# Performance work log

Measured on AMD Instinct MI355X. Metric: run time of the kernel, lower is better.

Reference implementation:

```python
import jax, jax.numpy as jnp
import numpy as np

N_NODES = 100000
N_EDGES = 1000000
N_LABEL = 200000
D_IN = 128
D_HID = 128


def setup_inputs() -> dict:
    key = jax.random.key(0)
    k1, k2, k3, k4, k5 = jax.random.split(key, 5)
    node_feature = jax.random.normal(k1, (N_NODES, D_IN), dtype=jnp.float32)
    edge_index = jax.random.randint(k2, (2, N_EDGES), 0, N_NODES, dtype=jnp.int64)
    edge_label_index = jax.random.randint(k3, (2, N_LABEL), 0, N_NODES, dtype=jnp.int64)
    W1 = jax.random.normal(k4, (D_IN, D_HID), dtype=jnp.float32) * (1.0 / np.sqrt(D_IN))
    b1 = jnp.zeros((D_HID,), dtype=jnp.float32)
    W2 = jax.random.normal(k5, (D_HID, D_HID), dtype=jnp.float32) * (1.0 / np.sqrt(D_HID))
    b2 = jnp.zeros((D_HID,), dtype=jnp.float32)
    return {"node_feature": node_feature, "edge_index": edge_index,
            "edge_label_index": edge_label_index,
            "W1": W1, "b1": b1, "W2": W2, "b2": b2}


def reference(node_feature, edge_index, edge_label_index, W1, b1, W2, b2):
    N = node_feature.shape[0]
    # GCN normalization with added self-loops (PyG GCNConv default)
    loop = jnp.arange(N, dtype=edge_index.dtype)
    src = jnp.concatenate([edge_index[0], loop])  # [E+N]
    dst = jnp.concatenate([edge_index[1], loop])  # [E+N]
    deg = jax.ops.segment_sum(jnp.ones_like(dst, dtype=node_feature.dtype), dst, N)
    dinv = jnp.where(deg > 0, jax.lax.rsqrt(deg), 0.0)
    norm = dinv[src] * dinv[dst]  # [E+N]

    def gcn_conv(x, W, b):
        h = x @ W                              # [N, d] transform first (d small)
        msg = h[src] * norm[:, None]           # gather + scale over edges
        return jax.ops.segment_sum(msg, dst, N) + b  # scatter-add to targets

    # eval mode: dropout(p=0.2) is identity
    x = jax.nn.relu(gcn_conv(node_feature, W1, b1))
    x = gcn_conv(x, W2, b2)

    # edge scoring: gather both endpoints, elementwise mul, sum over features
    nodes_first = x[edge_label_index[0]]
    nodes_second = x[edge_label_index[1]]
    pred = jnp.sum(nodes_first * nodes_second, axis=-1)  # [N_LABEL]
    return pred
```

## Files before the change

### kernel.cpp

```cpp
#include <hip/hip_runtime.h>
#include <hip/hip_bf16.h>


#define N_NODES 100000
#define N_EDGES 1000000
#define N_LABEL 200000
#define D_FEAT 128
#define BM 128

#define NB 782
#define BCAP 2048
#define P1_EPT 16
#define P1_BLOCKS 245
#define G_GEMM 782
#define G_CONV 128

typedef short bf16x8 __attribute__((ext_vector_type(8)));
typedef float f32x4 __attribute__((ext_vector_type(4)));

__device__ inline unsigned int f2bf(float x) {
    unsigned int u = __float_as_uint(x);
    return (u + 0x7FFFu + ((u >> 16) & 1u)) >> 16;
}
__device__ inline unsigned int bf16pack(float a, float b) {
    return f2bf(a) | (f2bf(b) << 16);
}
__device__ inline float bflo(unsigned int u) { return __uint_as_float(u << 16); }
__device__ inline float bfhi(unsigned int u) { return __uint_as_float(u & 0xFFFF0000u); }

__global__ __launch_bounds__(256) void w2bf_pass1(
    const float* __restrict__ W1, const float* __restrict__ W2,
    unsigned short* __restrict__ Wt1, unsigned short* __restrict__ Wt2,
    const int* __restrict__ src, const int* __restrict__ dst,
    unsigned int* __restrict__ temp, int* __restrict__ bofs) {
    __shared__ __align__(16) unsigned int S[4096 + 1024 + 256];
    int b = blockIdx.x, t = threadIdx.x;
    if (b < G_CONV) {
        int i = b * 256 + t;
        const float* W = (i < 16384) ? W1 : W2;
        unsigned short* Wt = (i < 16384) ? Wt1 : Wt2;
        int j = i & 16383;
        int n = j >> 7, k = j & 127;
        Wt[j] = (unsigned short)f2bf(W[(size_t)k * 128 + n]);
        return;
    }
    b -= G_CONV;
    unsigned int* ed16 = S;
    int* hist = (int*)(ed16 + 4096);
    int* red = hist + 1024;

    for (int i = t; i < 1024; i += 256) hist[i] = 0;
    __syncthreads();

    int se[P1_EPT], de[P1_EPT], rk[P1_EPT];
    int e0 = b * 4096 + t;
#pragma unroll
    for (int j = 0; j < P1_EPT; ++j) {
        int e = e0 + j * 256;
        if (e < N_EDGES) {
            se[j] = src[e];
            de[j] = dst[e];
            rk[j] = atomicAdd(&hist[de[j] >> 7], 1);
        }
    }
    __syncthreads();

    int c0 = hist[4 * t], c1 = hist[4 * t + 1], c2 = hist[4 * t + 2], c3 = hist[4 * t + 3];
    int s = c0 + c1 + c2 + c3;
    red[t] = s;
    __syncthreads();
    for (int off = 1; off < 256; off <<= 1) {
        int a = (t >= off) ? red[t - off] : 0;
        __syncthreads();
        red[t] += a;
        __syncthreads();
    }
    int excl = red[t] - s;
    hist[4 * t] = excl;
    hist[4 * t + 1] = excl + c0;
    hist[4 * t + 2] = excl + c0 + c1;
    hist[4 * t + 3] = excl + c0 + c1 + c2;
    __syncthreads();

#pragma unroll
    for (int j = 0; j < P1_EPT; ++j) {
        int e = e0 + j * 256;
        if (e < N_EDGES) {
            int pos = hist[de[j] >> 7] + rk[j];
            ed16[pos] = (unsigned int)(((de[j] & 127) << 17) | se[j]);
        }
    }
    __syncthreads();

#pragma unroll
    for (int i = 0; i < 4; ++i)
        ((uint4*)temp)[(size_t)b * 1024 + i * 256 + t] = ((uint4*)ed16)[i * 256 + t];
    for (int j = t; j < NB; j += 256) bofs[b * (NB + 1) + j] = hist[j];
    if (t == 0) {
        int cnt = N_EDGES - b * 4096;
        if (cnt > 4096) cnt = 4096;
        bofs[b * (NB + 1) + NB] = cnt;
    }
}

template <bool BF16_IN>
__device__ __forceinline__ void gemm_body(const void* __restrict__ Xv,
                                          const unsigned short* __restrict__ Wt,
                                          unsigned int* __restrict__ Y,
                                          int nrows, int bid, short* Ws) {
    int t = threadIdx.x;
#pragma unroll
    for (int i = 0; i < 8; ++i) {
        int c = i * 256 + t;
        int n = c >> 4, q = c & 15;
        uint4 v = *(const uint4*)&Wt[(size_t)n * 128 + q * 8];
        *(uint4*)&Ws[n * 128 + ((q ^ (n & 15)) << 3)] = v;
    }
    __syncthreads();

    int wv = t >> 6;
    int lane = t & 63, l16 = lane & 15, quad = lane >> 4;
    int rbase = bid * BM + wv * 32;

    f32x4 acc[2][8];
#pragma unroll
    for (int rt = 0; rt < 2; ++rt)
#pragma unroll
        for (int nt = 0; nt < 8; ++nt) acc[rt][nt] = (f32x4){0.f, 0.f, 0.f, 0.f};

#pragma unroll
    for (int kb = 0; kb < 4; ++kb) {
        bf16x8 af[2];
#pragma unroll
        for (int rt = 0; rt < 2; ++rt) {
            int row = rbase + rt * 16 + l16;
            if (row > nrows - 1) row = nrows - 1;
            if constexpr (BF16_IN) {
                const unsigned int* Xb = (const unsigned int*)Xv;
                af[rt] = *(const bf16x8*)&Xb[(size_t)row * 64 + kb * 16 + quad * 4];
            } else {
                const float* X = (const float*)Xv;
                float4 fa = ((const float4*)X)[(size_t)row * 32 + kb * 8 + quad * 2];
                float4 fb = ((const float4*)X)[(size_t)row * 32 + kb * 8 + quad * 2 + 1];
                union { uint4 u; bf16x8 v; } cv;
                cv.u.x = bf16pack(fa.x, fa.y);
                cv.u.y = bf16pack(fa.z, fa.w);
                cv.u.z = bf16pack(fb.x, fb.y);
                cv.u.w = bf16pack(fb.z, fb.w);
                af[rt] = cv.v;
            }
        }
        bf16x8 bfr[8];
#pragma unroll
        for (int nt = 0; nt < 8; ++nt) {
            int n = nt * 16 + l16;
            bfr[nt] = *(const bf16x8*)&Ws[n * 128 + (((kb * 4 + quad) ^ l16) << 3)];
        }
#pragma unroll
        for (int rt = 0; rt < 2; ++rt)
#pragma unroll
            for (int nt = 0; nt < 8; ++nt)
                acc[rt][nt] = __builtin_amdgcn_mfma_f32_16x16x32_bf16(
                    af[rt], bfr[nt], acc[rt][nt], 0, 0, 0);
    }

    short* Ys = (short*)Y;
#pragma unroll
    for (int rt = 0; rt < 2; ++rt)
#pragma unroll
        for (int reg = 0; reg < 4; ++reg) {
            int row = rbase + rt * 16 + quad * 4 + reg;
            if (row < nrows) {
#pragma unroll
                for (int nt = 0; nt < 8; ++nt)
                    Ys[(size_t)row * 128 + nt * 16 + l16] = (short)f2bf(acc[rt][nt][reg]);
            }
        }
}

__global__ __launch_bounds__(256) void gemm128_mfma_bf16(const unsigned int* __restrict__ Xb,
                                                         const unsigned short* __restrict__ Wt,
                                                         unsigned int* __restrict__ Y,
                                                         int nrows) {
    __shared__ __align__(16) short Ws[128 * 128];
    gemm_body<true>(Xb, Wt, Y, nrows, blockIdx.x, Ws);
}

__global__ __launch_bounds__(256) void fused_gemm1_pass2(
    const float* __restrict__ feat, const unsigned short* __restrict__ wt1,
    unsigned int* __restrict__ Hb,
    const unsigned int* __restrict__ temp, const int* __restrict__ bofs,
    int* __restrict__ row_ptr, float* __restrict__ dinv,
    int* __restrict__ packed) {
    __shared__ __align__(16) short Ws[128 * 128];
    int b = blockIdx.x, t = threadIdx.x;
    if (b < G_GEMM) {
        gemm_body<false>(feat, wt1, Hb, N_NODES, b, Ws);
        return;
    }
    int k = b - G_GEMM;
    unsigned int* ed = (unsigned int*)Ws;
    int* hist = (int*)(ed + BCAP);
    int* rp = hist + 128;
    int* cur = rp + 128;
    int* sc2 = cur + 128;
    int* red = sc2 + 128;
    int* sc = red + 256;

    int s_t = 0, len = 0;
    if (t < P1_BLOCKS) {
        s_t = bofs[t * (NB + 1) + k];
        len = bofs[t * (NB + 1) + k + 1] - s_t;
    }
    red[t] = s_t;
    __syncthreads();
    for (int off = 128; off > 0; off >>= 1) {
        if (t < off) red[t] += red[t + off];
        __syncthreads();
    }
    int gbase = red[0];
    __syncthreads();
    sc[t] = len;
    __syncthreads();
    for (int off = 1; off < 256; off <<= 1) {
        int a = (t >= off) ? sc[t - off] : 0;
        __syncthreads();
        sc[t] += a;
        __syncthreads();
    }
    int dloc = sc[t] - len;
    int nk = sc[255];
    if (nk > BCAP) nk = BCAP;

    if (t < 128) { hist[t] = 0; cur[t] = 0; }
    __syncthreads();
    for (int i = 0; i < len; ++i) {
        int d = dloc + i;
        if (d < BCAP) ed[d] = temp[(size_t)t * 4096 + s_t + i];
    }
    __syncthreads();
    for (int i = t; i < nk; i += 256) atomicAdd(&hist[ed[i] >> 17], 1);
    __syncthreads();

    if (t < 128) sc2[t] = hist[t];
    __syncthreads();
    for (int off = 1; off < 128; off <<= 1) {
        int a = (t < 128 && t >= off) ? sc2[t - off] : 0;
        __syncthreads();
        if (t < 128) sc2[t] += a;
        __syncthreads();
    }
    if (t < 128) {
        rp[t] = sc2[t] - hist[t];
        int n = k * 128 + t;
        if (n < N_NODES) {
            row_ptr[n] = gbase + rp[t];
            dinv[n] = rsqrtf((float)(hist[t] + 1));
        }
    }
    if (k == NB - 1 && t == 0) row_ptr[N_NODES] = N_EDGES;
    __syncthreads();

    for (int i = t; i < nk; i += 256) {
        unsigned int v = ed[i];
        int dl = v >> 17;
        int r = atomicAdd(&cur[dl], 1);
        packed[gbase + rp[dl] + r] = (int)(v & 0x1FFFF);
    }
}

template <bool RELU>
__global__ __launch_bounds__(256) void aggregate(const unsigned int* __restrict__ Hb,
                                                 const int* __restrict__ packed,
                                                 const int* __restrict__ row_ptr,
                                                 const float* __restrict__ dinv,
                                                 const float* __restrict__ bias,
                                                 unsigned int* __restrict__ Xb) {
    int v0 = blockIdx.x * 8 + (threadIdx.x >> 6) * 2;
    int v1 = v0 + 1;
    int lane = threadIdx.x & 63;
    if (v0 >= N_NODES) return;
    bool h1 = (v1 < N_NODES);

    int st0 = row_ptr[v0], en0 = row_ptr[v0 + 1];
    int st1 = h1 ? row_ptr[v1] : 0, en1 = h1 ? row_ptr[v1 + 1] : 0;
    float dv0 = dinv[v0];
    float dv1 = h1 ? dinv[v1] : 0.f;

    unsigned int su0 = Hb[(size_t)v0 * 64 + lane];
    float a0 = dv0 * bflo(su0), a1 = dv0 * bfhi(su0);
    unsigned int su1 = h1 ? Hb[(size_t)v1 * 64 + lane] : 0u;
    float b0 = dv1 * bflo(su1), b1 = dv1 * bfhi(su1);

    int p = 0;
    if (lane < 32) {
        if (st0 + lane < en0) p = packed[st0 + lane];
    } else {
        if (st1 + lane - 32 < en1) p = packed[st1 + lane - 32];
    }

    for (int c0 = st0, c1 = st1; c0 < en0 || c1 < en1; c0 += 32, c1 += 32) {
        int n0 = en0 - c0; n0 = n0 < 0 ? 0 : (n0 > 32 ? 32 : n0);
        int n1 = en1 - c1; n1 = n1 < 0 ? 0 : (n1 > 32 ? 32 : n1);
        bool act = (lane < 32) ? (lane < n0) : (lane - 32 < n1);
        float dld = dinv[p];
        float d = act ? dld : 0.f;

        int nmax = n0 > n1 ? n0 : n1;
        int pn = 0;
        bool pref = false;
        for (int j = 0; j < nmax; j += 8) {
            int sA[8], sB[8];
#pragma unroll
            for (int q = 0; q < 8; ++q) {
                sA[q] = __shfl(p, j + q);
                sB[q] = __shfl(p, 32 + j + q);
            }
            unsigned int uA[8], uB[8];
#pragma unroll
            for (int q = 0; q < 8; ++q) {
                uA[q] = Hb[(size_t)sA[q] * 64 + lane];
                uB[q] = Hb[(size_t)sB[q] * 64 + lane];
            }
            if (!pref) {
                pref = true;
                if (lane < 32) {
                    if (c0 + 32 + lane < en0) pn = packed[c0 + 32 + lane];
                } else {
                    if (c1 + lane < en1) pn = packed[c1 + lane];
                }
            }
            float dA[8], dB[8];
#pragma unroll
            for (int q = 0; q < 8; ++q) {
                dA[q] = __shfl(d, j + q);
                dB[q] = __shfl(d, 32 + j + q);
            }
#pragma unroll
            for (int q = 0; q < 8; ++q) {
                a0 = fmaf(dA[q], bflo(uA[q]), a0);
                a1 = fmaf(dA[q], bfhi(uA[q]), a1);
                b0 = fmaf(dB[q], bflo(uB[q]), b0);
                b1 = fmaf(dB[q], bfhi(uB[q]), b1);
            }
        }
        p = pn;
    }

    float2 bb = ((const float2*)bias)[lane];
    a0 = fmaf(a0, dv0, bb.x);
    a1 = fmaf(a1, dv0, bb.y);
    b0 = fmaf(b0, dv1, bb.x);
    b1 = fmaf(b1, dv1, bb.y);
    if (RELU) {
        a0 = fmaxf(a0, 0.f);
        a1 = fmaxf(a1, 0.f);
        b0 = fmaxf(b0, 0.f);
        b1 = fmaxf(b1, 0.f);
    }
    Xb[(size_t)v0 * 64 + lane] = bf16pack(a0, a1);
    if (h1) Xb[(size_t)v1 * 64 + lane] = bf16pack(b0, b1);
}

__global__ __launch_bounds__(256) void score_kernel(const int* __restrict__ ea,
                                                    const int* __restrict__ eb,
                                                    const unsigned int* __restrict__ Xb,
                                                    float* __restrict__ out) {
    int wbase = (blockIdx.x * 4 + (threadIdx.x >> 6)) * 4;
    int lane = threadIdx.x & 63;
    if (wbase >= N_LABEL) return;
    int ne = N_LABEL - wbase;
    if (ne > 4) ne = 4;

    unsigned int ua[4], ub[4];
#pragma unroll
    for (int e = 0; e < 4; ++e)
        if (e < ne) {
            int ia = ea[wbase + e], ib = eb[wbase + e];
            ua[e] = Xb[(size_t)ia * 64 + lane];
            ub[e] = Xb[(size_t)ib * 64 + lane];
        }
#pragma unroll
    for (int e = 0; e < 4; ++e)
        if (e < ne) {
            float p = bflo(ua[e]) * bflo(ub[e]) + bfhi(ua[e]) * bfhi(ub[e]);
#pragma unroll
            for (int off = 32; off > 0; off >>= 1) p += __shfl_down(p, off);
            if (lane == 0) out[wbase + e] = p;
        }
}

extern "C" void kernel_launch(void* const* d_in, const int* in_sizes, int n_in,
                              void* d_out, int out_size, void* d_ws, size_t ws_size,
                              hipStream_t stream) {
    const float* feat = (const float*)d_in[0];
    const int* ei = (const int*)d_in[1];
    const int* eli = (const int*)d_in[2];
    const float* W1 = (const float*)d_in[3];
    const float* b1 = (const float*)d_in[4];
    const float* W2 = (const float*)d_in[5];
    const float* b2 = (const float*)d_in[6];
    float* out = (float*)d_out;

    const int* src = ei;
    const int* dst = ei + N_EDGES;
    const int* la = eli;
    const int* lb = eli + N_LABEL;

    int* row_ptr = (int*)d_ws;
    float* dinv = (float*)(row_ptr + N_NODES + 4);
    unsigned short* wt1 = (unsigned short*)(dinv + N_NODES);
    unsigned short* wt2 = wt1 + 16384;
    int* packed = (int*)(wt2 + 16384);
    unsigned int* Hb = (unsigned int*)(packed + N_EDGES);
    unsigned int* Xb = Hb + (size_t)N_NODES * 64;
    unsigned int* temp = Xb;
    int* bofs = (int*)(temp + (size_t)P1_BLOCKS * 4096);

    const int TB = 256;
    int gGemm = (N_NODES + BM - 1) / BM;
    int gAgg = (N_NODES + 7) / 8;
    int gScore = (N_LABEL + 15) / 16;

    w2bf_pass1<<<G_CONV + P1_BLOCKS, TB, 0, stream>>>(W1, W2, wt1, wt2,
                                                      src, dst, temp, bofs);

    fused_gemm1_pass2<<<G_GEMM + NB, TB, 0, stream>>>(
        feat, wt1, Hb, temp, bofs, row_ptr, dinv, packed);

    aggregate<true><<<gAgg, TB, 0, stream>>>(Hb, packed, row_ptr, dinv, b1, Xb);

    gemm128_mfma_bf16<<<gGemm, TB, 0, stream>>>(Xb, wt2, Hb, N_NODES);
    aggregate<false><<<gAgg, TB, 0, stream>>>(Hb, packed, row_ptr, dinv, b2, Xb);

    score_kernel<<<gScore, TB, 0, stream>>>(la, lb, Xb, out);
}
```

Baseline: 275.5 us.

## Fuse aggregate, GEMM2, aggregate and scoring into one cooperative persistent kernel

Replaces the last four kernel launches with a single cooperative kernel. It loops over virtual blocks for each stage and uses grid-wide syncs between aggregate1, a half-width GEMM2 (N split into two 64-column halves held in LDS), aggregate2 and scoring. The aim is to remove launch gaps and tail effects between the short dependent kernels. In exchange it adds grid.sync barriers, a persistent grid sized by occupancy (with launch_bounds forcing 8 blocks per CU), and a GEMM that loads each A tile twice. The old path is kept as a fallback if the cooperative launch fails.

```diff
diff --git a/kernel.cpp b/kernel.cpp
--- a/kernel.cpp
+++ b/kernel.cpp
@@ -1,5 +1,8 @@
 #include <hip/hip_runtime.h>
 #include <hip/hip_bf16.h>
+#include <hip/hip_cooperative_groups.h>
+
+namespace cg = cooperative_groups;
 
 
 #define N_NODES 100000
@@ -14,6 +17,8 @@
 #define P1_BLOCKS 245
 #define G_GEMM 782
 #define G_CONV 128
+#define AGG_VB 12500
+#define SCORE_VB 12500
 
 typedef short bf16x8 __attribute__((ext_vector_type(8)));
 typedef float f32x4 __attribute__((ext_vector_type(4)));
@@ -270,13 +275,13 @@
 }
 
 template <bool RELU>
-__global__ __launch_bounds__(256) void aggregate(const unsigned int* __restrict__ Hb,
-                                                 const int* __restrict__ packed,
-                                                 const int* __restrict__ row_ptr,
-                                                 const float* __restrict__ dinv,
-                                                 const float* __restrict__ bias,
-                                                 unsigned int* __restrict__ Xb) {
-    int v0 = blockIdx.x * 8 + (threadIdx.x >> 6) * 2;
+__device__ __forceinline__ void agg_dev(int vb, const unsigned int* __restrict__ Hb,
+                                        const int* __restrict__ packed,
+                                        const int* __restrict__ row_ptr,
+                                        const float* __restrict__ dinv,
+                                        const float* __restrict__ bias,
+                                        unsigned int* __restrict__ Xb) {
+    int v0 = vb * 8 + (threadIdx.x >> 6) * 2;
     int v1 = v0 + 1;
     int lane = threadIdx.x & 63;
     if (v0 >= N_NODES) return;
@@ -362,11 +367,21 @@
     if (h1) Xb[(size_t)v1 * 64 + lane] = bf16pack(b0, b1);
 }
 
-__global__ __launch_bounds__(256) void score_kernel(const int* __restrict__ ea,
-                                                    const int* __restrict__ eb,
-                                                    const unsigned int* __restrict__ Xb,
-                                                    float* __restrict__ out) {
-    int wbase = (blockIdx.x * 4 + (threadIdx.x >> 6)) * 4;
+template <bool RELU>
+__global__ __launch_bounds__(256) void aggregate(const unsigned int* __restrict__ Hb,
+                                                 const int* __restrict__ packed,
+                                                 const int* __restrict__ row_ptr,
+                                                 const float* __restrict__ dinv,
+                                                 const float* __restrict__ bias,
+                                                 unsigned int* __restrict__ Xb) {
+    agg_dev<RELU>(blockIdx.x, Hb, packed, row_ptr, dinv, bias, Xb);
+}
+
+__device__ __forceinline__ void score_dev(int vb, const int* __restrict__ ea,
+                                          const int* __restrict__ eb,
+                                          const unsigned int* __restrict__ Xb,
+                                          float* __restrict__ out) {
+    int wbase = (vb * 4 + (threadIdx.x >> 6)) * 4;
     int lane = threadIdx.x & 63;
     if (wbase >= N_LABEL) return;
     int ne = N_LABEL - wbase;
@@ -388,6 +403,100 @@
             for (int off = 32; off > 0; off >>= 1) p += __shfl_down(p, off);
             if (lane == 0) out[wbase + e] = p;
         }
+}
+
+__global__ __launch_bounds__(256) void score_kernel(const int* __restrict__ ea,
+                                                    const int* __restrict__ eb,
+                                                    const unsigned int* __restrict__ Xb,
+                                                    float* __restrict__ out) {
+    score_dev(blockIdx.x, ea, eb, Xb, out);
+}
+
+__device__ __forceinline__ void gemm2half_dev(int vb, const unsigned int* __restrict__ Xb,
+                                              const unsigned short* __restrict__ Wt,
+                                              unsigned int* __restrict__ Y, short* Ws) {
+    int bid = vb >> 1, h = vb & 1;
+    int t = threadIdx.x;
+#pragma unroll
+    for (int i = 0; i < 4; ++i) {
+        int c = i * 256 + t;
+        int n = c >> 4, q = c & 15;
+        uint4 v = *(const uint4*)&Wt[(size_t)(h * 64 + n) * 128 + q * 8];
+        *(uint4*)&Ws[n * 128 + ((q ^ (n & 15)) << 3)] = v;
+    }
+    __syncthreads();
+
+    int wv = t >> 6;
+    int lane = t & 63, l16 = lane & 15, quad = lane >> 4;
+    int rbase = bid * BM + wv * 32;
+
+    f32x4 acc[2][4];
+#pragma unroll
+    for (int rt = 0; rt < 2; ++rt)
+#pragma unroll
+        for (int nt = 0; nt < 4; ++nt) acc[rt][nt] = (f32x4){0.f, 0.f, 0.f, 0.f};
+
+#pragma unroll
+    for (int kb = 0; kb < 4; ++kb) {
+        bf16x8 af[2];
+#pragma unroll
+        for (int rt = 0; rt < 2; ++rt) {
+            int row = rbase + rt * 16 + l16;
+            if (row > N_NODES - 1) row = N_NODES - 1;
+            af[rt] = *(const bf16x8*)&Xb[(size_t)row * 64 + kb * 16 + quad * 4];
+        }
+        bf16x8 bfr[4];
+#pragma unroll
+        for (int nt = 0; nt < 4; ++nt) {
+            int n = nt * 16 + l16;
+            bfr[nt] = *(const bf16x8*)&Ws[n * 128 + (((kb * 4 + quad) ^ l16) << 3)];
+        }
+#pragma unroll
+        for (int rt = 0; rt < 2; ++rt)
+#pragma unroll
+            for (int nt = 0; nt < 4; ++nt)
+                acc[rt][nt] = __builtin_amdgcn_mfma_f32_16x16x32_bf16(
+                    af[rt], bfr[nt], acc[rt][nt], 0, 0, 0);
+    }
+    __syncthreads();
+
+    short* Ys = (short*)Y;
+#pragma unroll
+    for (int rt = 0; rt < 2; ++rt)
+#pragma unroll
+        for (int reg = 0; reg < 4; ++reg) {
+            int row = rbase + rt * 16 + quad * 4 + reg;
+            if (row < N_NODES) {
+#pragma unroll
+                for (int nt = 0; nt < 4; ++nt)
+                    Ys[(size_t)row * 128 + h * 64 + nt * 16 + l16] =
+                        (short)f2bf(acc[rt][nt][reg]);
+            }
+        }
+}
+
+__global__ __launch_bounds__(256, 8) void tail_coop(
+    unsigned int* __restrict__ Hb, const int* __restrict__ packed,
+    const int* __restrict__ row_ptr, const float* __restrict__ dinv,
+    const float* __restrict__ b1, unsigned int* __restrict__ Xb,
+    const unsigned short* __restrict__ wt2, const float* __restrict__ b2,
+    const int* __restrict__ la, const int* __restrict__ lb,
+    float* __restrict__ out) {
+    __shared__ __align__(16) short Ws[64 * 128];
+    cg::grid_group grid = cg::this_grid();
+    int nb = gridDim.x;
+
+    for (int vb = blockIdx.x; vb < AGG_VB; vb += nb)
+        agg_dev<true>(vb, Hb, packed, row_ptr, dinv, b1, Xb);
+    grid.sync();
+    for (int vb = blockIdx.x; vb < 2 * G_GEMM; vb += nb)
+        gemm2half_dev(vb, Xb, wt2, Hb, Ws);
+    grid.sync();
+    for (int vb = blockIdx.x; vb < AGG_VB; vb += nb)
+        agg_dev<false>(vb, Hb, packed, row_ptr, dinv, b2, Xb);
+    grid.sync();
+    for (int vb = blockIdx.x; vb < SCORE_VB; vb += nb)
+        score_dev(vb, la, lb, Xb, out);
 }
 
 extern "C" void kernel_launch(void* const* d_in, const int* in_sizes, int n_in,
@@ -422,16 +531,44 @@
     int gAgg = (N_NODES + 7) / 8;
     int gScore = (N_LABEL + 15) / 16;
 
+    static int coop_grid = -2;
+    if (coop_grid == -2) {
+        int nb = 0;
+        hipError_t e1 = hipOccupancyMaxActiveBlocksPerMultiprocessor(&nb, tail_coop, 256, 0);
+        if (e1 != hipSuccess || nb < 1) {
+            coop_grid = -1;
+        } else {
+            int dev = 0;
+            hipGetDevice(&dev);
+            hipDeviceProp_t prop;
+            if (hipGetDeviceProperties(&prop, dev) != hipSuccess) {
+                coop_grid = -1;
+            } else {
+                long g = (long)nb * prop.multiProcessorCount;
+                coop_grid = (int)(g < AGG_VB ? g : AGG_VB);
+            }
+        }
+    }
+
     w2bf_pass1<<<G_CONV + P1_BLOCKS, TB, 0, stream>>>(W1, W2, wt1, wt2,
                                                       src, dst, temp, bofs);
 
     fused_gemm1_pass2<<<G_GEMM + NB, TB, 0, stream>>>(
         feat, wt1, Hb, temp, bofs, row_ptr, dinv, packed);
 
-    aggregate<true><<<gAgg, TB, 0, stream>>>(Hb, packed, row_ptr, dinv, b1, Xb);
-
-    gemm128_mfma_bf16<<<gGemm, TB, 0, stream>>>(Xb, wt2, Hb, N_NODES);
-    aggregate<false><<<gAgg, TB, 0, stream>>>(Hb, packed, row_ptr, dinv, b2, Xb);
-
-    score_kernel<<<gScore, TB, 0, stream>>>(la, lb, Xb, out);
-}
+    bool coop_ok = false;
+    if (coop_grid > 0) {
+        void* cargs[11] = {(void*)&Hb,     (void*)&packed, (void*)&row_ptr,
+                           (void*)&dinv,   (void*)&b1,     (void*)&Xb,
+                           (void*)&wt2,    (void*)&b2,     (void*)&la,
+                           (void*)&lb,     (void*)&out};
+        coop_ok = (hipLaunchCooperativeKernel(tail_coop, dim3(coop_grid), dim3(TB),
+                                              cargs, 0, stream) == hipSuccess);
+    }
+    if (!coop_ok) {
+        aggregate<true><<<gAgg, TB, 0, stream>>>(Hb, packed, row_ptr, dinv, b1, Xb);
+        gemm128_mfma_bf16<<<gGemm, TB, 0, stream>>>(Xb, wt2, Hb, N_NODES);
+        aggregate<false><<<gAgg, TB, 0, stream>>>(Hb, packed, row_ptr, dinv, b2, Xb);
+        score_kernel<<<gScore, TB, 0, stream>>>(la, lb, Xb, out);
+    }
+}
```

Result: slower. 845.3 us (+206.9%).
